# Performance work log

Hardware: AMD Instinct MI355X
Metric: run time of the kernel (lower is better)

Reference implementation:

```python
import jax, jax.numpy as jnp
import numpy as np

N = 50000   # nodes
E = 800000  # edges (avg degree 16)
D = 128     # feature / hidden dim


def _lin(x, W, b):
    # torch nn.Linear convention: W is [out, in]
    return x @ W.T + b


def setup_inputs() -> dict:
    key = jax.random.key(0)
    ks = jax.random.split(key, 24)
    p = lambda k, s: jax.random.normal(k, s, dtype=jnp.float32) * 0.05
    inp = {
        "node_feat": jax.random.normal(ks[0], (N, D), dtype=jnp.float32),
        "edge_feat": jax.random.normal(ks[1], (E, D), dtype=jnp.float32),
        "src_idx": jax.random.randint(ks[2], (E,), 0, N),
        "dst_idx": jax.random.randint(ks[3], (E,), 0, N),
        "Wsrc": p(ks[4], (D, D)), "bsrc": p(ks[5], (D,)),
        "Wdst": p(ks[6], (D, D)), "bdst": p(ks[7], (D,)),
        "Wphi1": p(ks[8], (D, D)), "bphi1": p(ks[9], (D,)),
        "Wphi2": p(ks[10], (D, D)), "bphi2": p(ks[11], (D,)),
        "Wphi3": p(ks[12], (D, D)), "bphi3": p(ks[13], (D,)),
        "Wth1": p(ks[14], (D, D)), "bth1": p(ks[15], (D,)),
        "Wth2": p(ks[16], (D, D)), "bth2": p(ks[17], (D,)),
        "Wpd": p(ks[18], (D, D)), "bpd": p(ks[19], (D,)),
        "Wpu": p(ks[20], (D, D)), "bpu": p(ks[21], (D,)),
    }
    return inp


def reference(node_feat, edge_feat, src_idx, dst_idx,
              Wsrc, bsrc, Wdst, bdst,
              Wphi1, bphi1, Wphi2, bphi2, Wphi3, bphi3,
              Wth1, bth1, Wth2, bth2,
              Wpd, bpd, Wpu, bpu):
    h = node_feat                               # [N, D]
    h_src = h[src_idx]                          # [E, D] gather
    h_dst = h[dst_idx]                          # [E, D] gather
    # edge code: e + affine(src) + affine(dst)
    t = edge_feat + _lin(h_src, Wsrc, bsrc) + _lin(h_dst, Wdst, bdst)
    # phi MLP (activation_first=True, n_hidden=2): ReLU, L, ReLU, L, ReLU, L
    x = jax.nn.relu(t)
    x = jax.nn.relu(_lin(x, Wphi1, bphi1))
    x = jax.nn.relu(_lin(x, Wphi2, bphi2))
    e_emb = _lin(x, Wphi3, bphi3)               # [E, D]
    # u_mul_e + sum: message = h[src] * e_emb, scatter-sum into dst
    m = h_src * e_emb                           # [E, D]
    agg = jax.ops.segment_sum(m, dst_idx, num_segments=h.shape[0])  # [N, D]
    # combine: theta(phi_dst(h) + phi_upd(agg)); theta = ReLU, L, ReLU, L
    y = _lin(h, Wpd, bpd) + _lin(agg, Wpu, bpu)
    y = jax.nn.relu(y)
    y = jax.nn.relu(_lin(y, Wth1, bth1))
    return _lin(y, Wth2, bth2)                  # [N, D]
```

## Files before the change

### kernel.cpp

```cpp
#include <hip/hip_runtime.h>
#include <hip/hip_bf16.h>

#define NN 50000
#define NE 800000
#define NT_E 12500
#define GRID_E 768
#define NBLK_SCAN 196

typedef __attribute__((ext_vector_type(8))) short bf16x8;
typedef __attribute__((ext_vector_type(4))) float f32x4;
typedef __attribute__((ext_vector_type(2))) float f32x2;
typedef __attribute__((ext_vector_type(8))) unsigned short u16x8;
typedef __attribute__((ext_vector_type(2))) unsigned short u16x2;

__device__ __forceinline__ unsigned short f2bf(float f) {
    union { float f; unsigned u; } v; v.f = f;
    unsigned r = v.u + 0x7FFFu + ((v.u >> 16) & 1u);
    return (unsigned short)(r >> 16);
}
__device__ __forceinline__ float bf2f(unsigned short h) {
    union { unsigned u; float f; } v; v.u = ((unsigned)h) << 16;
    return v.f;
}
__device__ __forceinline__ f32x4 mfma16(bf16x8 a, bf16x8 b, f32x4 c) {
    return __builtin_amdgcn_mfma_f32_16x16x32_bf16(a, b, c, 0, 0, 0);
}
__device__ __forceinline__ void syncl() {
    asm volatile("s_waitcnt lgkmcnt(0)\n\ts_barrier" ::: "memory");
}

__device__ __forceinline__ void load_wfrags(const unsigned short* __restrict__ Wb,
                                            int wv, int lane, bf16x8 (&wf)[4][2]) {
#pragma unroll
    for (int kk = 0; kk < 4; ++kk)
#pragma unroll
        for (int j = 0; j < 2; ++j) {
            int row = 32 * wv + 16 * j + (lane & 15);
            int col = 32 * kk + 8 * (lane >> 4);
            wf[kk][j] = *(const bf16x8*)(Wb + row * 128 + col);
        }
}

__device__ __forceinline__ void zero_acc(f32x4 (&acc)[4][2]) {
#pragma unroll
    for (int mt = 0; mt < 4; ++mt)
#pragma unroll
        for (int j = 0; j < 2; ++j) {
            f32x4 z = {0.f, 0.f, 0.f, 0.f};
            acc[mt][j] = z;
        }
}

__device__ __forceinline__ void gemm64(const unsigned short* __restrict__ X,
                                       const bf16x8 (&wf)[4][2], f32x4 (&acc)[4][2], int lane) {
#pragma unroll
    for (int kk = 0; kk < 4; ++kk) {
        bf16x8 a[4];
#pragma unroll
        for (int mt = 0; mt < 4; ++mt) {
            int row = mt * 16 + (lane & 15);
            a[mt] = *(const bf16x8*)(X + row * 136 + kk * 32 + 8 * (lane >> 4));
        }
#pragma unroll
        for (int mt = 0; mt < 4; ++mt) {
            acc[mt][0] = mfma16(a[mt], wf[kk][0], acc[mt][0]);
            acc[mt][1] = mfma16(a[mt], wf[kk][1], acc[mt][1]);
        }
    }
}

__device__ __forceinline__ void epi_lds(unsigned short* __restrict__ Xo,
                                        const f32x4 (&acc)[4][2],
                                        float bb0, float bb1, int c0, int rbase) {
#pragma unroll
    for (int mt = 0; mt < 4; ++mt)
#pragma unroll
        for (int r = 0; r < 4; ++r) {
            int row = mt * 16 + rbase + r;
            Xo[row * 136 + c0]      = f2bf(fmaxf(acc[mt][0][r] + bb0, 0.f));
            Xo[row * 136 + c0 + 16] = f2bf(fmaxf(acc[mt][1][r] + bb1, 0.f));
        }
}

__device__ __forceinline__ void stage_f32row(unsigned short* __restrict__ Xrow,
                                             const f32x4* __restrict__ p) {
#pragma unroll
    for (int i = 0; i < 4; ++i) {
        f32x4 lo = p[2 * i], hi = p[2 * i + 1];
        unsigned short tmp[8];
#pragma unroll
        for (int j = 0; j < 4; ++j) { tmp[j] = f2bf(lo[j]); tmp[4 + j] = f2bf(hi[j]); }
        *(u16x8*)(Xrow + i * 8) = *(u16x8*)tmp;
    }
}

__global__ void k_wconv(const float* w0, const float* w1, const float* w2,
                        const float* w3, const float* w4, const float* w5,
                        const float* w6, const float* w7, const float* w8,
                        unsigned short* out) {
    const float* ws[9] = {w0, w1, w2, w3, w4, w5, w6, w7, w8};
    int m = blockIdx.x >> 2;
    int part = blockIdx.x & 3;
    const float* w = ws[m] + part * 4096 + threadIdx.x * 16;
    unsigned short* o = out + m * 16384 + part * 4096 + threadIdx.x * 16;
    float f[16];
#pragma unroll
    for (int i = 0; i < 4; ++i) *(f32x4*)(f + 4 * i) = ((const f32x4*)w)[i];
    unsigned short tmp[16];
#pragma unroll
    for (int i = 0; i < 16; ++i) tmp[i] = f2bf(f[i]);
    ((u16x8*)o)[0] = *(u16x8*)tmp;
    ((u16x8*)o)[1] = *(u16x8*)(tmp + 8);
}

__global__ void k_hist(const int* __restrict__ dst, int* __restrict__ cnt) {
    int i = blockIdx.x * 256 + threadIdx.x;
    if (i < NE) atomicAdd(&cnt[dst[i]], 1);
}

__global__ void k_scan1(const int* __restrict__ c, int* __restrict__ bsum) {
    __shared__ int red[256];
    int i = blockIdx.x * 256 + threadIdx.x;
    red[threadIdx.x] = (i < NN) ? c[i] : 0;
    __syncthreads();
    for (int off = 128; off > 0; off >>= 1) {
        if (threadIdx.x < off) red[threadIdx.x] += red[threadIdx.x + off];
        __syncthreads();
    }
    if (threadIdx.x == 0) bsum[blockIdx.x] = red[0];
}

__global__ void k_scan2(int* __restrict__ bsum) {
    __shared__ int s[256];
    int t = threadIdx.x;
    s[t] = (t < NBLK_SCAN) ? bsum[t] : 0;
    __syncthreads();
    for (int off = 1; off < 256; off <<= 1) {
        int v = (t >= off) ? s[t - off] : 0;
        __syncthreads();
        s[t] += v;
        __syncthreads();
    }
    if (t < NBLK_SCAN) bsum[t] = (t == 0) ? 0 : s[t - 1];
}

__global__ void k_scan3(int* __restrict__ cnt, const int* __restrict__ bsum,
                        int* __restrict__ rowptr) {
    __shared__ int s[256];
    int t = threadIdx.x;
    int i = blockIdx.x * 256 + t;
    int v = (i < NN) ? cnt[i] : 0;
    s[t] = v;
    __syncthreads();
    for (int off = 1; off < 256; off <<= 1) {
        int x = (t >= off) ? s[t - off] : 0;
        __syncthreads();
        s[t] += x;
        __syncthreads();
    }
    int excl = bsum[blockIdx.x] + s[t] - v;
    if (i < NN) { rowptr[i] = excl; cnt[i] = excl; }
    if (i == 0) rowptr[NN] = NE;
}

__global__ void k_pos(const int* __restrict__ dst, int* __restrict__ cursor,
                      int* __restrict__ pos) {
    int i = blockIdx.x * 256 + threadIdx.x;
    if (i < NE) pos[i] = atomicAdd(&cursor[dst[i]], 1);
}

__global__ __launch_bounds__(256, 3)
void k_nodepre(const float* __restrict__ h,
               const unsigned short* __restrict__ Wb,
               const float* __restrict__ bsrc, const float* __restrict__ bdst,
               unsigned short* __restrict__ AH, unsigned short* __restrict__ Adst) {
    __shared__ unsigned short X[64 * 136];
    int tid = threadIdx.x, lane = tid & 63, wv = tid >> 6;
    int n0 = blockIdx.x * 64;
    {
        int row = tid >> 2, q = tid & 3;
        int n = n0 + row;
        if (n < NN) {
            unsigned short tmp[32];
            const f32x4* hp = (const f32x4*)(h + (size_t)n * 128 + q * 32);
#pragma unroll
            for (int i = 0; i < 8; ++i) {
                f32x4 v = hp[i];
#pragma unroll
                for (int j = 0; j < 4; ++j) tmp[i * 4 + j] = f2bf(v[j]);
            }
#pragma unroll
            for (int i = 0; i < 4; ++i)
                *(u16x8*)(X + row * 136 + q * 32 + i * 8) = *(u16x8*)(tmp + i * 8);
            u16x8* hb = (u16x8*)(AH + (size_t)n * 256 + 128 + q * 32);
#pragma unroll
            for (int i = 0; i < 4; ++i) hb[i] = *(u16x8*)(tmp + i * 8);
        } else {
            u16x8 z = {0, 0, 0, 0, 0, 0, 0, 0};
#pragma unroll
            for (int i = 0; i < 4; ++i) *(u16x8*)(X + row * 136 + q * 32 + i * 8) = z;
        }
    }
    __syncthreads();

    bf16x8 wfS[4][2], wfD[4][2];
    load_wfrags(Wb, wv, lane, wfS);
    load_wfrags(Wb + 16384, wv, lane, wfD);
    f32x4 accS[4][2], accD[4][2];
    zero_acc(accS); zero_acc(accD);
    gemm64(X, wfS, accS, lane);
    gemm64(X, wfD, accD, lane);

    int c0 = 32 * wv + (lane & 15);
    float bs0 = bsrc[c0], bs1 = bsrc[c0 + 16];
    float bd0 = bdst[c0], bd1 = bdst[c0 + 16];
    int rbase = (lane >> 4) * 4;
#pragma unroll
    for (int mt = 0; mt < 4; ++mt)
#pragma unroll
        for (int r = 0; r < 4; ++r) {
            int n = n0 + mt * 16 + rbase + r;
            if (n < NN) {
                AH[(size_t)n * 256 + c0]        = f2bf(accS[mt][0][r] + bs0);
                AH[(size_t)n * 256 + c0 + 16]   = f2bf(accS[mt][1][r] + bs1);
                Adst[(size_t)n * 128 + c0]      = f2bf(accD[mt][0][r] + bd0);
                Adst[(size_t)n * 128 + c0 + 16] = f2bf(accD[mt][1][r] + bd1);
            }
        }
}

__global__ __launch_bounds__(256, 3)
void k_edgeB(const float* __restrict__ ef,
             const int* __restrict__ src, const int* __restrict__ dst,
             const int* __restrict__ pos,
             const unsigned short* __restrict__ AH,
             const unsigned short* __restrict__ Adst,
             const unsigned short* __restrict__ Wb,
             const float* __restrict__ b1, const float* __restrict__ b2,
             const float* __restrict__ b3,
             unsigned short* __restrict__ Mbuf) {
    __shared__ __align__(16) char sh[52480];
    unsigned short* X0 = (unsigned short*)sh;
    unsigned short* X1 = (unsigned short*)(sh + 17408);
    unsigned short* Hs = (unsigned short*)(sh + 34816);
    float*          Mf = (float*)sh;
    int*         posarr = (int*)(sh + 52224);

    int tid = threadIdx.x, lane = tid & 63, wv = tid >> 6;

    bf16x8 wf1[4][2], wf2[4][2];
    load_wfrags(Wb + 2 * 16384, wv, lane, wf1);
    load_wfrags(Wb + 3 * 16384, wv, lane, wf2);

    int c0 = 32 * wv + (lane & 15);
    float b1_0 = b1[c0], b1_1 = b1[c0 + 16];
    float b2_0 = b2[c0], b2_1 = b2[c0 + 16];
    float b3_0 = b3[c0], b3_1 = b3[c0 + 16];
    int rbase = (lane >> 4) * 4;
    int srow = tid >> 2, q = tid & 3;

    int b = blockIdx.x, nb = gridDim.x;
    int qt = NT_E / nb, rt = NT_E % nb;
    int t0 = (b < rt) ? b * (qt + 1) : rt * (qt + 1) + (b - rt) * qt;
    int t1 = t0 + ((b < rt) ? qt + 1 : qt);

    for (int t = t0; t < t1; ++t) {
        int e0 = t * 64;
        syncl();
        {
            int e = e0 + srow;
            int s = src[e], d = dst[e];
            if (q == 0) posarr[srow] = pos[e];
            const f32x4* ep = (const f32x4*)(ef + (size_t)e * 128 + q * 32);
            const u16x8* ap = (const u16x8*)(AH + (size_t)s * 256 + q * 32);
            const u16x8* hp = (const u16x8*)(AH + (size_t)s * 256 + 128 + q * 32);
            const u16x8* dp = (const u16x8*)(Adst + (size_t)d * 128 + q * 32);
#pragma unroll
            for (int i = 0; i < 4; ++i) {
                u16x8 a8 = ap[i], d8 = dp[i], h8 = hp[i];
                f32x4 lo = ep[2 * i], hi = ep[2 * i + 1];
                unsigned short o[8];
#pragma unroll
                for (int j = 0; j < 8; ++j) {
                    float evv = (j < 4) ? lo[j] : hi[j - 4];
                    float v = evv + bf2f((unsigned short)a8[j]) + bf2f((unsigned short)d8[j]);
                    o[j] = f2bf(fmaxf(v, 0.f));
                }
                *(u16x8*)(X0 + srow * 136 + q * 32 + i * 8) = *(u16x8*)o;
                *(u16x8*)(Hs + srow * 136 + q * 32 + i * 8) = h8;
            }
        }
        syncl();
        f32x4 acc[4][2];
        zero_acc(acc);
        gemm64(X0, wf1, acc, lane);
        syncl();
        epi_lds(X1, acc, b1_0, b1_1, c0, rbase);
        syncl();
        zero_acc(acc);
        gemm64(X1, wf2, acc, lane);
        epi_lds(X0, acc, b2_0, b2_1, c0, rbase);
        syncl();
        bf16x8 wf3[4][2];
        load_wfrags(Wb + 4 * 16384, wv, lane, wf3);
        zero_acc(acc);
        gemm64(X0, wf3, acc, lane);
        syncl();
#pragma unroll
        for (int mt = 0; mt < 4; ++mt)
#pragma unroll
            for (int r = 0; r < 4; ++r) {
                int row = mt * 16 + rbase + r;
                float h0 = bf2f(Hs[row * 136 + c0]);
                float h1 = bf2f(Hs[row * 136 + c0 + 16]);
                Mf[row * 128 + c0]      = (acc[mt][0][r] + b3_0) * h0;
                Mf[row * 128 + c0 + 16] = (acc[mt][1][r] + b3_1) * h1;
            }
        syncl();
#pragma unroll
        for (int i = 0; i < 16; ++i) {
            int row = wv * 16 + i;
            int posr = posarr[row];
            f32x2 v = *(const f32x2*)(Mf + row * 128 + lane * 2);
            u16x2 o2; o2[0] = f2bf(v[0]); o2[1] = f2bf(v[1]);
            *(u16x2*)(Mbuf + (size_t)posr * 128 + lane * 2) = o2;
        }
    }
}

__global__ __launch_bounds__(256)
void k_agg(const unsigned short* __restrict__ Mbuf,
           const int* __restrict__ rowptr, float* __restrict__ agg) {
    int n = (blockIdx.x * 256 + threadIdx.x) >> 6;
    int lane = threadIdx.x & 63;
    if (n >= NN) return;
    int j0 = rowptr[n], j1 = rowptr[n + 1];
    float a0 = 0.f, a1 = 0.f;
    int j = j0;
    for (; j + 3 < j1; j += 4) {
        u16x2 v0 = *(const u16x2*)(Mbuf + (size_t)j * 128 + lane * 2);
        u16x2 v1 = *(const u16x2*)(Mbuf + (size_t)(j + 1) * 128 + lane * 2);
        u16x2 v2 = *(const u16x2*)(Mbuf + (size_t)(j + 2) * 128 + lane * 2);
        u16x2 v3 = *(const u16x2*)(Mbuf + (size_t)(j + 3) * 128 + lane * 2);
        a0 += bf2f(v0[0]) + bf2f(v1[0]) + bf2f(v2[0]) + bf2f(v3[0]);
        a1 += bf2f(v0[1]) + bf2f(v1[1]) + bf2f(v2[1]) + bf2f(v3[1]);
    }
    for (; j < j1; ++j) {
        u16x2 v = *(const u16x2*)(Mbuf + (size_t)j * 128 + lane * 2);
        a0 += bf2f(v[0]); a1 += bf2f(v[1]);
    }
    f32x2 o; o[0] = a0; o[1] = a1;
    *(f32x2*)(agg + (size_t)n * 128 + lane * 2) = o;
}

__global__ __launch_bounds__(256, 2)
void k_edge_atomic(const float* __restrict__ ef,
                   const int* __restrict__ src, const int* __restrict__ dst,
                   const unsigned short* __restrict__ AH,
                   const unsigned short* __restrict__ Adst,
                   const unsigned short* __restrict__ Wb,
                   const float* __restrict__ b1, const float* __restrict__ b2,
                   const float* __restrict__ b3,
                   float* __restrict__ agg) {
    __shared__ unsigned short X0[64 * 136];
    __shared__ unsigned short X1[64 * 136];
    __shared__ unsigned short Hs[64 * 136];
    __shared__ int doff_lds[64];

    int tid = threadIdx.x, lane = tid & 63, wv = tid >> 6;
    bf16x8 wf1[4][2], wf2[4][2], wf3[4][2];
    load_wfrags(Wb + 2 * 16384, wv, lane, wf1);
    load_wfrags(Wb + 3 * 16384, wv, lane, wf2);
    load_wfrags(Wb + 4 * 16384, wv, lane, wf3);

    int c0 = 32 * wv + (lane & 15);
    float b1_0 = b1[c0], b1_1 = b1[c0 + 16];
    float b2_0 = b2[c0], b2_1 = b2[c0 + 16];
    float b3_0 = b3[c0], b3_1 = b3[c0 + 16];
    int rbase = (lane >> 4) * 4;
    int srow = tid >> 2, q = tid & 3;

    for (int t = blockIdx.x; t < NT_E; t += gridDim.x) {
        int e0 = t * 64;
        __syncthreads();
        {
            int e = e0 + srow;
            int s = src[e], d = dst[e];
            if (q == 0) doff_lds[srow] = d * 128;
            const f32x4* ep = (const f32x4*)(ef + (size_t)e * 128 + q * 32);
            const u16x8* ap = (const u16x8*)(AH + (size_t)s * 256 + q * 32);
            const u16x8* hp = (const u16x8*)(AH + (size_t)s * 256 + 128 + q * 32);
            const u16x8* dp = (const u16x8*)(Adst + (size_t)d * 128 + q * 32);
#pragma unroll
            for (int i = 0; i < 4; ++i) {
                u16x8 a8 = ap[i], d8 = dp[i], h8 = hp[i];
                f32x4 lo = ep[2 * i], hi = ep[2 * i + 1];
                unsigned short o[8];
#pragma unroll
                for (int j = 0; j < 8; ++j) {
                    float evv = (j < 4) ? lo[j] : hi[j - 4];
                    float v = evv + bf2f((unsigned short)a8[j]) + bf2f((unsigned short)d8[j]);
                    o[j] = f2bf(fmaxf(v, 0.f));
                }
                *(u16x8*)(X0 + srow * 136 + q * 32 + i * 8) = *(u16x8*)o;
                *(u16x8*)(Hs + srow * 136 + q * 32 + i * 8) = h8;
            }
        }
        __syncthreads();
        f32x4 acc[4][2];
        zero_acc(acc);
        gemm64(X0, wf1, acc, lane);
        __syncthreads();
        epi_lds(X1, acc, b1_0, b1_1, c0, rbase);
        __syncthreads();
        zero_acc(acc);
        gemm64(X1, wf2, acc, lane);
        epi_lds(X0, acc, b2_0, b2_1, c0, rbase);
        __syncthreads();
        zero_acc(acc);
        gemm64(X0, wf3, acc, lane);
#pragma unroll
        for (int mt = 0; mt < 4; ++mt)
#pragma unroll
            for (int r = 0; r < 4; ++r) {
                int row = mt * 16 + rbase + r;
                int dofs = doff_lds[row];
                float h0 = bf2f(Hs[row * 136 + c0]);
                float h1 = bf2f(Hs[row * 136 + c0 + 16]);
                atomicAdd(agg + dofs + c0,      (acc[mt][0][r] + b3_0) * h0);
                atomicAdd(agg + dofs + c0 + 16, (acc[mt][1][r] + b3_1) * h1);
            }
    }
}

__global__ __launch_bounds__(256, 3)
void k_nodeout(const unsigned short* __restrict__ AH,
               const float* __restrict__ agg,
               const unsigned short* __restrict__ Wb,
               const float* __restrict__ bpd, const float* __restrict__ bpu,
               const float* __restrict__ bt1, const float* __restrict__ bt2,
               float* __restrict__ out) {
    __shared__ unsigned short Xh[64 * 136];
    __shared__ unsigned short Xa[64 * 136];
    int tid = threadIdx.x, lane = tid & 63, wv = tid >> 6;
    int n0 = blockIdx.x * 64;
    {
        int row = tid >> 2, q = tid & 3;
        int n = n0 + row;
        if (n < NN) {
            const u16x8* hp = (const u16x8*)(AH + (size_t)n * 256 + 128 + q * 32);
#pragma unroll
            for (int i = 0; i < 4; ++i)
                *(u16x8*)(Xh + row * 136 + q * 32 + i * 8) = hp[i];
            stage_f32row(Xa + row * 136 + q * 32,
                         (const f32x4*)(agg + (size_t)n * 128 + q * 32));
        } else {
            u16x8 z = {0, 0, 0, 0, 0, 0, 0, 0};
#pragma unroll
            for (int i = 0; i < 4; ++i) {
                *(u16x8*)(Xh + row * 136 + q * 32 + i * 8) = z;
                *(u16x8*)(Xa + row * 136 + q * 32 + i * 8) = z;
            }
        }
    }
    __syncthreads();
    bf16x8 wfa[4][2], wfb[4][2];
    load_wfrags(Wb + 5 * 16384, wv, lane, wfa);
    load_wfrags(Wb + 6 * 16384, wv, lane, wfb);
    int c0 = 32 * wv + (lane & 15);
    int rbase = (lane >> 4) * 4;
    f32x4 acc[4][2];
    zero_acc(acc);
    gemm64(Xh, wfa, acc, lane);
    gemm64(Xa, wfb, acc, lane);
    float bb0 = bpd[c0] + bpu[c0], bb1 = bpd[c0 + 16] + bpu[c0 + 16];
    __syncthreads();
    epi_lds(Xh, acc, bb0, bb1, c0, rbase);
    __syncthreads();
    load_wfrags(Wb + 7 * 16384, wv, lane, wfa);
    zero_acc(acc);
    gemm64(Xh, wfa, acc, lane);
    float b10 = bt1[c0], b11 = bt1[c0 + 16];
    __syncthreads();
    epi_lds(Xa, acc, b10, b11, c0, rbase);
    __syncthreads();
    load_wfrags(Wb + 8 * 16384, wv, lane, wfb);
    zero_acc(acc);
    gemm64(Xa, wfb, acc, lane);
    float b20 = bt2[c0], b21 = bt2[c0 + 16];
#pragma unroll
    for (int mt = 0; mt < 4; ++mt)
#pragma unroll
        for (int r = 0; r < 4; ++r) {
            int n = n0 + mt * 16 + rbase + r;
            if (n < NN) {
                out[(size_t)n * 128 + c0]      = acc[mt][0][r] + b20;
                out[(size_t)n * 128 + c0 + 16] = acc[mt][1][r] + b21;
            }
        }
}

extern "C" void kernel_launch(void* const* d_in, const int* in_sizes, int n_in,
                              void* d_out, int out_size, void* d_ws, size_t ws_size,
                              hipStream_t stream) {
    (void)in_sizes; (void)n_in; (void)out_size;
    const float* node_feat = (const float*)d_in[0];
    const float* edge_feat = (const float*)d_in[1];
    const int*   src  = (const int*)d_in[2];
    const int*   dst  = (const int*)d_in[3];
    const float* Wsrc = (const float*)d_in[4];  const float* bsrc = (const float*)d_in[5];
    const float* Wdst = (const float*)d_in[6];  const float* bdst = (const float*)d_in[7];
    const float* Wphi1 = (const float*)d_in[8]; const float* bphi1 = (const float*)d_in[9];
    const float* Wphi2 = (const float*)d_in[10];const float* bphi2 = (const float*)d_in[11];
    const float* Wphi3 = (const float*)d_in[12];const float* bphi3 = (const float*)d_in[13];
    const float* Wth1 = (const float*)d_in[14]; const float* bth1 = (const float*)d_in[15];
    const float* Wth2 = (const float*)d_in[16]; const float* bth2 = (const float*)d_in[17];
    const float* Wpd  = (const float*)d_in[18]; const float* bpd  = (const float*)d_in[19];
    const float* Wpu  = (const float*)d_in[20]; const float* bpu  = (const float*)d_in[21];

    char* ws = (char*)d_ws;
    size_t off = 0;
    unsigned short* Wb   = (unsigned short*)(ws + off); off += 294912;
    unsigned short* AH   = (unsigned short*)(ws + off); off += 25600000;
    unsigned short* Adst = (unsigned short*)(ws + off); off += 12800000;
    float*          agg  = (float*)(ws + off);          off += 25600000;
    int*            cnt  = (int*)(ws + off);            off += 200064;
    int*            rowptr = (int*)(ws + off);          off += 200064;
    int*            bsum = (int*)(ws + off);            off += 1024;
    int*            pos  = (int*)(ws + off);            off += 3200000;
    unsigned short* Mbuf = (unsigned short*)(ws + off); off += 204800000;
    bool primary = (ws_size >= off);

    k_wconv<<<36, 256, 0, stream>>>(Wsrc, Wdst, Wphi1, Wphi2, Wphi3,
                                    Wpd, Wpu, Wth1, Wth2, Wb);
    k_nodepre<<<782, 256, 0, stream>>>(node_feat, Wb, bsrc, bdst, AH, Adst);

    if (primary) {
        hipMemsetAsync(cnt, 0, (size_t)NN * 4, stream);
        k_hist<<<3125, 256, 0, stream>>>(dst, cnt);
        k_scan1<<<NBLK_SCAN, 256, 0, stream>>>(cnt, bsum);
        k_scan2<<<1, 256, 0, stream>>>(bsum);
        k_scan3<<<NBLK_SCAN, 256, 0, stream>>>(cnt, bsum, rowptr);
        k_pos<<<3125, 256, 0, stream>>>(dst, cnt, pos);
        k_edgeB<<<GRID_E, 256, 0, stream>>>(edge_feat, src, dst, pos,
                                            AH, Adst, Wb,
                                            bphi1, bphi2, bphi3, Mbuf);
        k_agg<<<12500, 256, 0, stream>>>(Mbuf, rowptr, agg);
    } else {
        hipMemsetAsync(agg, 0, (size_t)NN * 128 * 4, stream);
        k_edge_atomic<<<1024, 256, 0, stream>>>(edge_feat, src, dst,
                                                AH, Adst, Wb,
                                                bphi1, bphi2, bphi3, agg);
    }
    k_nodeout<<<782, 256, 0, stream>>>(AH, agg, Wb, bpd, bpu, bth1, bth2,
                                       (float*)d_out);
}
```

Measured before the change: 510.9 us.

## Fuse segment-sum into node output kernel and slim edge kernel LDS for occupancy

The separate aggregation kernel is removed. Its CSR segment-sum now runs inside a new node-output kernel that stages the aggregated rows in LDS and feeds them straight into the combine and theta GEMMs, so the fp32 agg array no longer makes a round trip through global memory. The edge kernel drops its Hs and Mf LDS buffers by holding h_src in registers and writing the message from a bf16 LDS tile. It also loads weight fragments per GEMM rather than keeping them live, which allows 4 blocks per CU and a larger grid. The cost is that per-row messages are now rounded to bf16 before the multiply, and the aggregation in the fused kernel serializes over 16 rows per wave.

```diff
diff --git a/kernel.cpp b/kernel.cpp
--- a/kernel.cpp
+++ b/kernel.cpp
@@ -4,7 +4,7 @@
 #define NN 50000
 #define NE 800000
 #define NT_E 12500
-#define GRID_E 768
+#define GRID_E 1024
 #define NBLK_SCAN 196
 
 typedef __attribute__((ext_vector_type(8))) short bf16x8;
@@ -79,6 +79,19 @@
             int row = mt * 16 + rbase + r;
             Xo[row * 136 + c0]      = f2bf(fmaxf(acc[mt][0][r] + bb0, 0.f));
             Xo[row * 136 + c0 + 16] = f2bf(fmaxf(acc[mt][1][r] + bb1, 0.f));
+        }
+}
+
+__device__ __forceinline__ void epi_lds_norelu(unsigned short* __restrict__ Xo,
+                                               const f32x4 (&acc)[4][2],
+                                               float bb0, float bb1, int c0, int rbase) {
+#pragma unroll
+    for (int mt = 0; mt < 4; ++mt)
+#pragma unroll
+        for (int r = 0; r < 4; ++r) {
+            int row = mt * 16 + rbase + r;
+            Xo[row * 136 + c0]      = f2bf(acc[mt][0][r] + bb0);
+            Xo[row * 136 + c0 + 16] = f2bf(acc[mt][1][r] + bb1);
         }
 }
 
@@ -229,7 +242,7 @@
         }
 }
 
-__global__ __launch_bounds__(256, 3)
+__global__ __launch_bounds__(256, 4)
 void k_edgeB(const float* __restrict__ ef,
              const int* __restrict__ src, const int* __restrict__ dst,
              const int* __restrict__ pos,
@@ -239,18 +252,12 @@
              const float* __restrict__ b1, const float* __restrict__ b2,
              const float* __restrict__ b3,
              unsigned short* __restrict__ Mbuf) {
-    __shared__ __align__(16) char sh[52480];
+    __shared__ __align__(16) char sh[35072];
     unsigned short* X0 = (unsigned short*)sh;
     unsigned short* X1 = (unsigned short*)(sh + 17408);
-    unsigned short* Hs = (unsigned short*)(sh + 34816);
-    float*          Mf = (float*)sh;
-    int*         posarr = (int*)(sh + 52224);
+    int*         posarr = (int*)(sh + 34816);
 
     int tid = threadIdx.x, lane = tid & 63, wv = tid >> 6;
-
-    bf16x8 wf1[4][2], wf2[4][2];
-    load_wfrags(Wb + 2 * 16384, wv, lane, wf1);
-    load_wfrags(Wb + 3 * 16384, wv, lane, wf2);
 
     int c0 = 32 * wv + (lane & 15);
     float b1_0 = b1[c0], b1_1 = b1[c0 + 16];
@@ -266,6 +273,7 @@
 
     for (int t = t0; t < t1; ++t) {
         int e0 = t * 64;
+        u16x8 hbr[4];
         syncl();
         {
             int e = e0 + srow;
@@ -277,7 +285,8 @@
             const u16x8* dp = (const u16x8*)(Adst + (size_t)d * 128 + q * 32);
 #pragma unroll
             for (int i = 0; i < 4; ++i) {
-                u16x8 a8 = ap[i], d8 = dp[i], h8 = hp[i];
+                u16x8 a8 = ap[i], d8 = dp[i];
+                hbr[i] = hp[i];
                 f32x4 lo = ep[2 * i], hi = ep[2 * i + 1];
                 unsigned short o[8];
 #pragma unroll
@@ -287,70 +296,140 @@
                     o[j] = f2bf(fmaxf(v, 0.f));
                 }
                 *(u16x8*)(X0 + srow * 136 + q * 32 + i * 8) = *(u16x8*)o;
-                *(u16x8*)(Hs + srow * 136 + q * 32 + i * 8) = h8;
             }
         }
         syncl();
         f32x4 acc[4][2];
-        zero_acc(acc);
-        gemm64(X0, wf1, acc, lane);
+        {
+            bf16x8 wf[4][2];
+            load_wfrags(Wb + 2 * 16384, wv, lane, wf);
+            zero_acc(acc);
+            gemm64(X0, wf, acc, lane);
+        }
         syncl();
         epi_lds(X1, acc, b1_0, b1_1, c0, rbase);
         syncl();
-        zero_acc(acc);
-        gemm64(X1, wf2, acc, lane);
+        {
+            bf16x8 wf[4][2];
+            load_wfrags(Wb + 3 * 16384, wv, lane, wf);
+            zero_acc(acc);
+            gemm64(X1, wf, acc, lane);
+        }
         epi_lds(X0, acc, b2_0, b2_1, c0, rbase);
         syncl();
-        bf16x8 wf3[4][2];
-        load_wfrags(Wb + 4 * 16384, wv, lane, wf3);
-        zero_acc(acc);
-        gemm64(X0, wf3, acc, lane);
+        {
+            bf16x8 wf[4][2];
+            load_wfrags(Wb + 4 * 16384, wv, lane, wf);
+            zero_acc(acc);
+            gemm64(X0, wf, acc, lane);
+        }
         syncl();
-#pragma unroll
-        for (int mt = 0; mt < 4; ++mt)
-#pragma unroll
-            for (int r = 0; r < 4; ++r) {
-                int row = mt * 16 + rbase + r;
-                float h0 = bf2f(Hs[row * 136 + c0]);
-                float h1 = bf2f(Hs[row * 136 + c0 + 16]);
-                Mf[row * 128 + c0]      = (acc[mt][0][r] + b3_0) * h0;
-                Mf[row * 128 + c0 + 16] = (acc[mt][1][r] + b3_1) * h1;
-            }
+        epi_lds_norelu(X1, acc, b3_0, b3_1, c0, rbase);
         syncl();
-#pragma unroll
-        for (int i = 0; i < 16; ++i) {
-            int row = wv * 16 + i;
-            int posr = posarr[row];
-            f32x2 v = *(const f32x2*)(Mf + row * 128 + lane * 2);
-            u16x2 o2; o2[0] = f2bf(v[0]); o2[1] = f2bf(v[1]);
-            *(u16x2*)(Mbuf + (size_t)posr * 128 + lane * 2) = o2;
-        }
-    }
-}
-
-__global__ __launch_bounds__(256)
-void k_agg(const unsigned short* __restrict__ Mbuf,
-           const int* __restrict__ rowptr, float* __restrict__ agg) {
-    int n = (blockIdx.x * 256 + threadIdx.x) >> 6;
-    int lane = threadIdx.x & 63;
-    if (n >= NN) return;
-    int j0 = rowptr[n], j1 = rowptr[n + 1];
-    float a0 = 0.f, a1 = 0.f;
-    int j = j0;
-    for (; j + 3 < j1; j += 4) {
-        u16x2 v0 = *(const u16x2*)(Mbuf + (size_t)j * 128 + lane * 2);
-        u16x2 v1 = *(const u16x2*)(Mbuf + (size_t)(j + 1) * 128 + lane * 2);
-        u16x2 v2 = *(const u16x2*)(Mbuf + (size_t)(j + 2) * 128 + lane * 2);
-        u16x2 v3 = *(const u16x2*)(Mbuf + (size_t)(j + 3) * 128 + lane * 2);
-        a0 += bf2f(v0[0]) + bf2f(v1[0]) + bf2f(v2[0]) + bf2f(v3[0]);
-        a1 += bf2f(v0[1]) + bf2f(v1[1]) + bf2f(v2[1]) + bf2f(v3[1]);
-    }
-    for (; j < j1; ++j) {
-        u16x2 v = *(const u16x2*)(Mbuf + (size_t)j * 128 + lane * 2);
-        a0 += bf2f(v[0]); a1 += bf2f(v[1]);
-    }
-    f32x2 o; o[0] = a0; o[1] = a1;
-    *(f32x2*)(agg + (size_t)n * 128 + lane * 2) = o;
+        {
+            int posr = posarr[srow];
+            unsigned short* mp = Mbuf + (size_t)posr * 128 + q * 32;
+#pragma unroll
+            for (int i = 0; i < 4; ++i) {
+                u16x8 ev = *(const u16x8*)(X1 + srow * 136 + q * 32 + i * 8);
+                u16x8 o;
+#pragma unroll
+                for (int j = 0; j < 8; ++j)
+                    o[j] = f2bf(bf2f((unsigned short)ev[j]) * bf2f((unsigned short)hbr[i][j]));
+                *(u16x8*)(mp + i * 8) = o;
+            }
+        }
+    }
+}
+
+__global__ __launch_bounds__(256, 3)
+void k_nodeoutF(const unsigned short* __restrict__ AH,
+                const unsigned short* __restrict__ Mbuf,
+                const int* __restrict__ rowptr,
+                const unsigned short* __restrict__ Wb,
+                const float* __restrict__ bpd, const float* __restrict__ bpu,
+                const float* __restrict__ bt1, const float* __restrict__ bt2,
+                float* __restrict__ out) {
+    __shared__ unsigned short Xh[64 * 136];
+    __shared__ unsigned short Xa[64 * 136];
+    int tid = threadIdx.x, lane = tid & 63, wv = tid >> 6;
+    int n0 = blockIdx.x * 64;
+    {
+        int row = tid >> 2, q = tid & 3;
+        int n = n0 + row;
+        if (n < NN) {
+            const u16x8* hp = (const u16x8*)(AH + (size_t)n * 256 + 128 + q * 32);
+#pragma unroll
+            for (int i = 0; i < 4; ++i)
+                *(u16x8*)(Xh + row * 136 + q * 32 + i * 8) = hp[i];
+        } else {
+            u16x8 z = {0, 0, 0, 0, 0, 0, 0, 0};
+#pragma unroll
+            for (int i = 0; i < 4; ++i)
+                *(u16x8*)(Xh + row * 136 + q * 32 + i * 8) = z;
+        }
+    }
+    {
+#pragma unroll 1
+        for (int it = 0; it < 16; ++it) {
+            int row = wv * 16 + it;
+            int n = n0 + row;
+            float a0 = 0.f, a1 = 0.f;
+            if (n < NN) {
+                int j0 = rowptr[n], j1 = rowptr[n + 1];
+                int j = j0;
+                for (; j + 3 < j1; j += 4) {
+                    u16x2 v0 = *(const u16x2*)(Mbuf + (size_t)j * 128 + lane * 2);
+                    u16x2 v1 = *(const u16x2*)(Mbuf + (size_t)(j + 1) * 128 + lane * 2);
+                    u16x2 v2 = *(const u16x2*)(Mbuf + (size_t)(j + 2) * 128 + lane * 2);
+                    u16x2 v3 = *(const u16x2*)(Mbuf + (size_t)(j + 3) * 128 + lane * 2);
+                    a0 += bf2f(v0[0]) + bf2f(v1[0]) + bf2f(v2[0]) + bf2f(v3[0]);
+                    a1 += bf2f(v0[1]) + bf2f(v1[1]) + bf2f(v2[1]) + bf2f(v3[1]);
+                }
+                for (; j < j1; ++j) {
+                    u16x2 v = *(const u16x2*)(Mbuf + (size_t)j * 128 + lane * 2);
+                    a0 += bf2f(v[0]); a1 += bf2f(v[1]);
+                }
+            }
+            Xa[row * 136 + lane * 2]     = f2bf(a0);
+            Xa[row * 136 + lane * 2 + 1] = f2bf(a1);
+        }
+    }
+    __syncthreads();
+    bf16x8 wfa[4][2], wfb[4][2];
+    load_wfrags(Wb + 5 * 16384, wv, lane, wfa);
+    load_wfrags(Wb + 6 * 16384, wv, lane, wfb);
+    int c0 = 32 * wv + (lane & 15);
+    int rbase = (lane >> 4) * 4;
+    f32x4 acc[4][2];
+    zero_acc(acc);
+    gemm64(Xh, wfa, acc, lane);
+    gemm64(Xa, wfb, acc, lane);
+    float bb0 = bpd[c0] + bpu[c0], bb1 = bpd[c0 + 16] + bpu[c0 + 16];
+    __syncthreads();
+    epi_lds(Xh, acc, bb0, bb1, c0, rbase);
+    __syncthreads();
+    load_wfrags(Wb + 7 * 16384, wv, lane, wfa);
+    zero_acc(acc);
+    gemm64(Xh, wfa, acc, lane);
+    float b10 = bt1[c0], b11 = bt1[c0 + 16];
+    __syncthreads();
+    epi_lds(Xa, acc, b10, b11, c0, rbase);
+    __syncthreads();
+    load_wfrags(Wb + 8 * 16384, wv, lane, wfb);
+    zero_acc(acc);
+    gemm64(Xa, wfb, acc, lane);
+    float b20 = bt2[c0], b21 = bt2[c0 + 16];
+#pragma unroll
+    for (int mt = 0; mt < 4; ++mt)
+#pragma unroll
+        for (int r = 0; r < 4; ++r) {
+            int n = n0 + mt * 16 + rbase + r;
+            if (n < NN) {
+                out[(size_t)n * 128 + c0]      = acc[mt][0][r] + b20;
+                out[(size_t)n * 128 + c0 + 16] = acc[mt][1][r] + b21;
+            }
+        }
 }
 
 __global__ __launch_bounds__(256, 2)
@@ -545,13 +624,14 @@
         k_edgeB<<<GRID_E, 256, 0, stream>>>(edge_feat, src, dst, pos,
                                             AH, Adst, Wb,
                                             bphi1, bphi2, bphi3, Mbuf);
-        k_agg<<<12500, 256, 0, stream>>>(Mbuf, rowptr, agg);
+        k_nodeoutF<<<782, 256, 0, stream>>>(AH, Mbuf, rowptr, Wb,
+                                            bpd, bpu, bth1, bth2, (float*)d_out);
     } else {
         hipMemsetAsync(agg, 0, (size_t)NN * 128 * 4, stream);
         k_edge_atomic<<<1024, 256, 0, stream>>>(edge_feat, src, dst,
                                                 AH, Adst, Wb,
                                                 bphi1, bphi2, bphi3, agg);
-    }
-    k_nodeout<<<782, 256, 0, stream>>>(AH, agg, Wb, bpd, bpu, bth1, bth2,
-                                       (float*)d_out);
-}
+        k_nodeout<<<782, 256, 0, stream>>>(AH, agg, Wb, bpd, bpu, bth1, bth2,
+                                           (float*)d_out);
+    }
+}
```

Result: slower. 536.2 us (+5.0%).
